# Kernel optimization log

Hardware: AMD Instinct MI355X
Metric: run time of the kernel (lower is better)

The kernel has to match this reference:

```python
import jax, jax.numpy as jnp
import numpy as np

WINDOW = 12
NUM_HEADS = 16

def window_partition(x, ws):
    b, h, w, c = x.shape
    x = x.reshape(b, h // ws, ws, w // ws, ws, c)
    return x.transpose(0, 1, 3, 2, 4, 5).reshape(-1, ws, ws, c)

def window_reverse(windows, ws, h, w):
    c = windows.shape[-1]
    x = windows.reshape(-1, h // ws, w // ws, ws, ws, c)
    return x.transpose(0, 1, 3, 2, 4, 5).reshape(-1, h, w, c)

def setup_inputs() -> dict:
    key = jax.random.key(0)
    ks = jax.random.split(key, 5)
    dim = 512
    hidden_states = jax.random.normal(ks[0], (8, 48, 48, dim), dtype=jnp.float32)
    qkv_w = jax.random.normal(ks[1], (dim, 3 * dim), dtype=jnp.float32) * 0.02
    qkv_b = jnp.zeros((3 * dim,), dtype=jnp.float32)
    proj_w = jax.random.normal(ks[2], (dim, dim), dtype=jnp.float32) * 0.02
    proj_b = jnp.zeros((dim,), dtype=jnp.float32)
    return {"hidden_states": hidden_states, "qkv_w": qkv_w, "qkv_b": qkv_b,
            "proj_w": proj_w, "proj_b": proj_b}

def reference(hidden_states, qkv_w, qkv_b, proj_w, proj_b):
    b, h, w, c = hidden_states.shape
    ws = WINDOW
    nh = NUM_HEADS
    hd = c // nh
    scale = hd ** -0.5
    pad_r = (ws - w % ws) % ws
    pad_b = (ws - h % ws) % ws
    x = jnp.pad(hidden_states, ((0, 0), (0, pad_b), (0, pad_r), (0, 0)))
    ph, pw = x.shape[1], x.shape[2]
    # [nW, ws*ws, C]
    xw = window_partition(x, ws).reshape(-1, ws * ws, c)
    nw, nt, _ = xw.shape
    qkv = (xw @ qkv_w + qkv_b).reshape(nw, nt, 3, nh, hd)
    qkv = qkv.transpose(2, 0, 3, 1, 4)  # [3, nW, nh, nt, hd]
    q, k, v = qkv[0], qkv[1], qkv[2]
    scores = jnp.einsum('wnqd,wnkd->wnqk', q, k) * scale
    attn = jax.nn.softmax(scores, axis=-1)
    out = jnp.einsum('wnqk,wnkd->wnqd', attn, v)  # [nW, nh, nt, hd]
    out = out.transpose(0, 2, 1, 3).reshape(nw, nt, c)
    out = out @ proj_w + proj_b
    out = out.reshape(-1, ws, ws, c)
    out = window_reverse(out, ws, ph, pw)
    out = out[:, :h, :w, :]
    return out.reshape(b, h * w, c)
```

## Files before the change

### kernel.cpp

```cpp
#include <hip/hip_runtime.h>
#include <hip/hip_bf16.h>


typedef unsigned short u16;
typedef unsigned int u32;
typedef __attribute__((ext_vector_type(4))) float f32x4;
typedef __attribute__((ext_vector_type(8))) short short8;

#define MFMA16(a, b, c) __builtin_amdgcn_mfma_f32_16x16x32_bf16(a, b, c, 0, 0, 0)

__device__ __forceinline__ u16 f2b(float f) {
  __hip_bfloat16 h = __float2bfloat16(f);
  return *reinterpret_cast<u16*>(&h);
}

__global__ void prep_x_kernel(const float* __restrict__ x, u16* __restrict__ xw) {
  int c = blockIdx.x * 256 + threadIdx.x;
  int r = c >> 6;
  int colb = (c & 63) << 3;
  int win = r / 144, tok = r - win * 144;
  int b = win >> 4, wh = (win >> 2) & 3, ww = win & 3;
  int i = tok / 12, j = tok - i * 12;
  const float* src = x + ((size_t)((b * 48 + wh * 12 + i) * 48 + ww * 12 + j)) * 512 + colb;
  float4 a0 = *(const float4*)(src);
  float4 a1 = *(const float4*)(src + 4);
  short8 o;
  o[0] = (short)f2b(a0.x); o[1] = (short)f2b(a0.y); o[2] = (short)f2b(a0.z); o[3] = (short)f2b(a0.w);
  o[4] = (short)f2b(a1.x); o[5] = (short)f2b(a1.y); o[6] = (short)f2b(a1.z); o[7] = (short)f2b(a1.w);
  *reinterpret_cast<short8*>(xw + (size_t)r * 512 + colb) = o;
}

__global__ void prep_wt_kernel(const float* __restrict__ w, u16* __restrict__ wt,
                               int K, int N) {
  int t = blockIdx.x * 256 + threadIdx.x;
  int nchunks = N >> 3;
  if (t >= K * nchunks) return;
  int k = t / nchunks;
  int n0 = (t - k * nchunks) << 3;
  const float* src = w + (size_t)k * N + n0;
  float4 a0 = *(const float4*)(src);
  float4 a1 = *(const float4*)(src + 4);
  float v[8] = {a0.x, a0.y, a0.z, a0.w, a1.x, a1.y, a1.z, a1.w};
#pragma unroll
  for (int j = 0; j < 8; j++) wt[(size_t)(n0 + j) * K + k] = f2b(v[j]);
}

template <int EPI>
__global__ __launch_bounds__(256) void gemm_bt_kernel(
    const u16* __restrict__ A, const u16* __restrict__ BT,
    const float* __restrict__ bias,
    u16* __restrict__ outb, float* __restrict__ outf,
    int M, int N, int K) {
  __shared__ __align__(16) u16 sA[128 * 64];
  __shared__ __align__(16) u16 sB[128 * 64];
  const int tid = threadIdx.x;
  const int wave = tid >> 6;
  const int lane = tid & 63;
  const int bm = blockIdx.x;
  const int bn = blockIdx.y;
  const int wr = (wave >> 1) << 6;
  const int wc = (wave & 1) << 6;
  const int l15 = lane & 15;
  const int lhi = lane >> 4;

  f32x4 acc[4][4];
  const f32x4 fzero = {0.f, 0.f, 0.f, 0.f};
#pragma unroll
  for (int i = 0; i < 4; i++)
#pragma unroll
    for (int j = 0; j < 4; j++) acc[i][j] = fzero;

  const int srow = lane >> 3;
  const int scol = (lane & 7) << 3;
  const u16* Abase = A + (size_t)(bm * 128) * K;
  const u16* Bbase = BT + (size_t)(bn * 128) * K;

  for (int k0 = 0; k0 < K; k0 += 64) {
#pragma unroll
    for (int i = 0; i < 4; ++i) {
      const int chunk = wave * 4 + i;
      const int row = chunk * 8 + srow;
      __builtin_amdgcn_global_load_lds(
          (const __attribute__((address_space(1))) u32*)(Abase + (size_t)row * K + k0 + scol),
          (__attribute__((address_space(3))) u32*)(sA + chunk * 512), 16, 0, 0);
      __builtin_amdgcn_global_load_lds(
          (const __attribute__((address_space(1))) u32*)(Bbase + (size_t)row * K + k0 + scol),
          (__attribute__((address_space(3))) u32*)(sB + chunk * 512), 16, 0, 0);
    }
    __syncthreads();

    short8 af[4][2], bfr[4][2];
#pragma unroll
    for (int t = 0; t < 4; t++) {
#pragma unroll
      for (int kk = 0; kk < 2; kk++) {
        af[t][kk]  = *reinterpret_cast<const short8*>(sA + (wr + t * 16 + l15) * 64 + kk * 32 + lhi * 8);
        bfr[t][kk] = *reinterpret_cast<const short8*>(sB + (wc + t * 16 + l15) * 64 + kk * 32 + lhi * 8);
      }
    }
#pragma unroll
    for (int kk = 0; kk < 2; kk++)
#pragma unroll
      for (int i = 0; i < 4; i++)
#pragma unroll
        for (int j = 0; j < 4; j++)
          acc[i][j] = MFMA16(af[i][kk], bfr[j][kk], acc[i][j]);
    __syncthreads();
  }

#pragma unroll
  for (int i = 0; i < 4; i++) {
    const int rowbase = bm * 128 + wr + i * 16 + lhi * 4;
#pragma unroll
    for (int j = 0; j < 4; j++) {
      const int col = bn * 128 + wc + j * 16 + l15;
      const float bv = bias[col];
#pragma unroll
      for (int r = 0; r < 4; r++) {
        float v = acc[i][j][r] + bv;
        int row = rowbase + r;
        if (EPI == 0) {
          outb[(size_t)row * N + col] = f2b(v);
        } else {
          int win = row / 144, tok = row - win * 144;
          int b = win >> 4, wh = (win >> 2) & 3, ww = win & 3;
          int ii = tok / 12, jj = tok - ii * 12;
          size_t o = ((size_t)b * 2304 + (wh * 12 + ii) * 48 + (ww * 12 + jj)) * 512 + col;
          outf[o] = v;
        }
      }
    }
  }
}

__global__ __launch_bounds__(192) void attn_kernel(const u16* __restrict__ qkv,
                                                   u16* __restrict__ outb) {
  constexpr int PSTR = 168;
  __shared__ __align__(16) u16 sP[3 * 48 * PSTR];
  __shared__ __align__(16) u16 sVT[32 * PSTR];
  const int tid = threadIdx.x;
  const int wave = tid >> 6;
  const int lane = tid & 63;
  const int l15 = lane & 15;
  const int lhi = lane >> 4;
  const int win = blockIdx.x;
  const int head = blockIdx.y;
  const size_t base = ((size_t)win * 144) * 1536 + head * 32;
  const u16* Q = qkv + base;
  const u16* Kp = qkv + base + 512;
  const u16* V = qkv + base + 1024;
  constexpr float SCALE = 0.17677669529663687f;
  const f32x4 fzero = {0.f, 0.f, 0.f, 0.f};

  for (int t = tid; t < 576; t += 192) {
    int tok = t >> 2, dblk = t & 3;
    short8 v = *reinterpret_cast<const short8*>(V + (size_t)tok * 1536 + dblk * 8);
#pragma unroll
    for (int j = 0; j < 8; j++) sVT[(dblk * 8 + j) * PSTR + tok] = (u16)v[j];
  }
  for (int t = tid; t < 512; t += 192) {
    int d = t >> 4, cc = 144 + (t & 15);
    sVT[d * PSTR + cc] = 0;
  }
  u16* sPw = sP + wave * 48 * PSTR;
  for (int t = lane; t < 768; t += 64) {
    int rr = t >> 4, cc = 144 + (t & 15);
    sPw[rr * PSTR + cc] = 0;
  }

  short8 qa[3];
#pragma unroll
  for (int mt = 0; mt < 3; mt++) {
    int row = wave * 48 + mt * 16 + l15;
    qa[mt] = *reinterpret_cast<const short8*>(Q + (size_t)row * 1536 + lhi * 8);
  }

  f32x4 s[3][9];
#pragma unroll
  for (int nt = 0; nt < 9; nt++) {
    int ctok = nt * 16 + l15;
    short8 kb = *reinterpret_cast<const short8*>(Kp + (size_t)ctok * 1536 + lhi * 8);
#pragma unroll
    for (int mt = 0; mt < 3; mt++) s[mt][nt] = MFMA16(qa[mt], kb, fzero);
  }

#pragma unroll
  for (int mt = 0; mt < 3; mt++) {
#pragma unroll
    for (int r = 0; r < 4; r++) {
      float m = -1e30f;
#pragma unroll
      for (int nt = 0; nt < 9; nt++) m = fmaxf(m, s[mt][nt][r]);
#pragma unroll
      for (int off = 1; off < 16; off <<= 1) m = fmaxf(m, __shfl_xor(m, off, 64));
      float p[9], sum = 0.f;
#pragma unroll
      for (int nt = 0; nt < 9; nt++) {
        p[nt] = __expf((s[mt][nt][r] - m) * SCALE);
        sum += p[nt];
      }
#pragma unroll
      for (int off = 1; off < 16; off <<= 1) sum += __shfl_xor(sum, off, 64);
      float inv = 1.f / sum;
      int prow = mt * 16 + lhi * 4 + r;
#pragma unroll
      for (int nt = 0; nt < 9; nt++)
        sPw[prow * PSTR + nt * 16 + l15] = f2b(p[nt] * inv);
    }
  }

  __syncthreads();

  f32x4 o[3][2];
#pragma unroll
  for (int mt = 0; mt < 3; mt++)
#pragma unroll
    for (int nt = 0; nt < 2; nt++) o[mt][nt] = fzero;
#pragma unroll
  for (int kk = 0; kk < 5; kk++) {
    short8 pa[3];
#pragma unroll
    for (int mt = 0; mt < 3; mt++)
      pa[mt] = *reinterpret_cast<const short8*>(sPw + (mt * 16 + l15) * PSTR + kk * 32 + lhi * 8);
#pragma unroll
    for (int nt = 0; nt < 2; nt++) {
      short8 vb = *reinterpret_cast<const short8*>(sVT + (nt * 16 + l15) * PSTR + kk * 32 + lhi * 8);
#pragma unroll
      for (int mt = 0; mt < 3; mt++) o[mt][nt] = MFMA16(pa[mt], vb, o[mt][nt]);
    }
  }

  const int rowb = win * 144 + wave * 48;
#pragma unroll
  for (int mt = 0; mt < 3; mt++) {
#pragma unroll
    for (int nt = 0; nt < 2; nt++) {
      int col = head * 32 + nt * 16 + l15;
#pragma unroll
      for (int r = 0; r < 4; r++) {
        int row = rowb + mt * 16 + lhi * 4 + r;
        outb[(size_t)row * 512 + col] = f2b(o[mt][nt][r]);
      }
    }
  }
}

extern "C" void kernel_launch(void* const* d_in, const int* in_sizes, int n_in,
                              void* d_out, int out_size, void* d_ws, size_t ws_size,
                              hipStream_t stream) {
  const float* x      = (const float*)d_in[0];
  const float* qkv_w  = (const float*)d_in[1];
  const float* qkv_b  = (const float*)d_in[2];
  const float* proj_w = (const float*)d_in[3];
  const float* proj_b = (const float*)d_in[4];
  float* out = (float*)d_out;

  u16* xw     = (u16*)d_ws;
  u16* qkvT   = xw + (size_t)18432 * 512;
  u16* projT  = qkvT + (size_t)1536 * 512;
  u16* qkvout = projT + (size_t)512 * 512;
  u16* attno  = qkvout + (size_t)18432 * 1536;

  prep_x_kernel<<<4608, 256, 0, stream>>>(x, xw);
  prep_wt_kernel<<<384, 256, 0, stream>>>(qkv_w, qkvT, 512, 1536);
  prep_wt_kernel<<<128, 256, 0, stream>>>(proj_w, projT, 512, 512);

  gemm_bt_kernel<0><<<dim3(144, 12), 256, 0, stream>>>(
      xw, qkvT, qkv_b, qkvout, nullptr, 18432, 1536, 512);

  attn_kernel<<<dim3(128, 16), 192, 0, stream>>>(qkvout, attno);

  gemm_bt_kernel<1><<<dim3(144, 4), 256, 0, stream>>>(
      attno, projT, proj_b, nullptr, out, 18432, 512, 512);
}
```

Baseline: 226.9 us.

## Swizzle GEMM LDS tiles and stream attention per row-tile to cut LDS and registers

The GEMM now XOR-swizzles the 16-byte chunk column by row when writing to and reading from LDS, which is meant to avoid bank conflicts on the MFMA operand loads. The attention kernel computes QK, softmax and PV for one 16-row tile at a time, reusing a per-wave P buffer one third the size. This reduces LDS footprint and live score registers, which may allow more blocks per CU. It also switches to exp2f with a prescaled log2e constant. Reusing the P buffer relies on intra-wave ordering of LDS writes and reads with no barrier, which is a correctness risk.

```diff
diff --git a/kernel.cpp b/kernel.cpp
--- a/kernel.cpp
+++ b/kernel.cpp
@@ -71,7 +71,7 @@
     for (int j = 0; j < 4; j++) acc[i][j] = fzero;
 
   const int srow = lane >> 3;
-  const int scol = (lane & 7) << 3;
+  const int scol = (((lane & 7) ^ srow) << 3);
   const u16* Abase = A + (size_t)(bm * 128) * K;
   const u16* Bbase = BT + (size_t)(bn * 128) * K;
 
@@ -94,8 +94,12 @@
     for (int t = 0; t < 4; t++) {
 #pragma unroll
       for (int kk = 0; kk < 2; kk++) {
-        af[t][kk]  = *reinterpret_cast<const short8*>(sA + (wr + t * 16 + l15) * 64 + kk * 32 + lhi * 8);
-        bfr[t][kk] = *reinterpret_cast<const short8*>(sB + (wc + t * 16 + l15) * 64 + kk * 32 + lhi * 8);
+        const int rA = wr + t * 16 + l15;
+        const int rB = wc + t * 16 + l15;
+        const int cA = (kk * 32 + lhi * 8) ^ ((rA & 7) << 3);
+        const int cB = (kk * 32 + lhi * 8) ^ ((rB & 7) << 3);
+        af[t][kk]  = *reinterpret_cast<const short8*>(sA + rA * 64 + cA);
+        bfr[t][kk] = *reinterpret_cast<const short8*>(sB + rB * 64 + cB);
       }
     }
 #pragma unroll
@@ -136,8 +140,8 @@
 __global__ __launch_bounds__(192) void attn_kernel(const u16* __restrict__ qkv,
                                                    u16* __restrict__ outb) {
   constexpr int PSTR = 168;
-  __shared__ __align__(16) u16 sP[3 * 48 * PSTR];
   __shared__ __align__(16) u16 sVT[32 * PSTR];
+  __shared__ __align__(16) u16 sP[3 * 16 * PSTR];
   const int tid = threadIdx.x;
   const int wave = tid >> 6;
   const int lane = tid & 63;
@@ -149,7 +153,7 @@
   const u16* Q = qkv + base;
   const u16* Kp = qkv + base + 512;
   const u16* V = qkv + base + 1024;
-  constexpr float SCALE = 0.17677669529663687f;
+  constexpr float SC2 = 0.25509915922608635f;
   const f32x4 fzero = {0.f, 0.f, 0.f, 0.f};
 
   for (int t = tid; t < 576; t += 192) {
@@ -162,10 +166,12 @@
     int d = t >> 4, cc = 144 + (t & 15);
     sVT[d * PSTR + cc] = 0;
   }
-  u16* sPw = sP + wave * 48 * PSTR;
-  for (int t = lane; t < 768; t += 64) {
-    int rr = t >> 4, cc = 144 + (t & 15);
-    sPw[rr * PSTR + cc] = 0;
+  u16* sPw = sP + wave * 16 * PSTR;
+  {
+    for (int t = lane; t < 256; t += 64) {
+      int rr = t >> 4, cc = 144 + (t & 15);
+      sPw[rr * PSTR + cc] = 0;
+    }
   }
 
   short8 qa[3];
@@ -174,59 +180,57 @@
     int row = wave * 48 + mt * 16 + l15;
     qa[mt] = *reinterpret_cast<const short8*>(Q + (size_t)row * 1536 + lhi * 8);
   }
-
-  f32x4 s[3][9];
+  short8 kb[9];
 #pragma unroll
   for (int nt = 0; nt < 9; nt++) {
     int ctok = nt * 16 + l15;
-    short8 kb = *reinterpret_cast<const short8*>(Kp + (size_t)ctok * 1536 + lhi * 8);
-#pragma unroll
-    for (int mt = 0; mt < 3; mt++) s[mt][nt] = MFMA16(qa[mt], kb, fzero);
-  }
+    kb[nt] = *reinterpret_cast<const short8*>(Kp + (size_t)ctok * 1536 + lhi * 8);
+  }
+
+  __syncthreads();
+
+  f32x4 o[3][2];
+#pragma unroll
+  for (int mt = 0; mt < 3; mt++)
+#pragma unroll
+    for (int nt = 0; nt < 2; nt++) o[mt][nt] = fzero;
 
 #pragma unroll
   for (int mt = 0; mt < 3; mt++) {
+    f32x4 s[9];
+#pragma unroll
+    for (int nt = 0; nt < 9; nt++) s[nt] = MFMA16(qa[mt], kb[nt], fzero);
+
 #pragma unroll
     for (int r = 0; r < 4; r++) {
       float m = -1e30f;
 #pragma unroll
-      for (int nt = 0; nt < 9; nt++) m = fmaxf(m, s[mt][nt][r]);
+      for (int nt = 0; nt < 9; nt++) m = fmaxf(m, s[nt][r]);
 #pragma unroll
       for (int off = 1; off < 16; off <<= 1) m = fmaxf(m, __shfl_xor(m, off, 64));
       float p[9], sum = 0.f;
 #pragma unroll
       for (int nt = 0; nt < 9; nt++) {
-        p[nt] = __expf((s[mt][nt][r] - m) * SCALE);
+        p[nt] = exp2f((s[nt][r] - m) * SC2);
         sum += p[nt];
       }
 #pragma unroll
       for (int off = 1; off < 16; off <<= 1) sum += __shfl_xor(sum, off, 64);
       float inv = 1.f / sum;
-      int prow = mt * 16 + lhi * 4 + r;
+      int prow = lhi * 4 + r;
 #pragma unroll
       for (int nt = 0; nt < 9; nt++)
         sPw[prow * PSTR + nt * 16 + l15] = f2b(p[nt] * inv);
     }
-  }
-
-  __syncthreads();
-
-  f32x4 o[3][2];
-#pragma unroll
-  for (int mt = 0; mt < 3; mt++)
-#pragma unroll
-    for (int nt = 0; nt < 2; nt++) o[mt][nt] = fzero;
-#pragma unroll
-  for (int kk = 0; kk < 5; kk++) {
-    short8 pa[3];
-#pragma unroll
-    for (int mt = 0; mt < 3; mt++)
-      pa[mt] = *reinterpret_cast<const short8*>(sPw + (mt * 16 + l15) * PSTR + kk * 32 + lhi * 8);
-#pragma unroll
-    for (int nt = 0; nt < 2; nt++) {
-      short8 vb = *reinterpret_cast<const short8*>(sVT + (nt * 16 + l15) * PSTR + kk * 32 + lhi * 8);
-#pragma unroll
-      for (int mt = 0; mt < 3; mt++) o[mt][nt] = MFMA16(pa[mt], vb, o[mt][nt]);
+
+#pragma unroll
+    for (int kk = 0; kk < 5; kk++) {
+      short8 pa = *reinterpret_cast<const short8*>(sPw + l15 * PSTR + kk * 32 + lhi * 8);
+#pragma unroll
+      for (int nt = 0; nt < 2; nt++) {
+        short8 vb = *reinterpret_cast<const short8*>(sVT + (nt * 16 + l15) * PSTR + kk * 32 + lhi * 8);
+        o[mt][nt] = MFMA16(pa, vb, o[mt][nt]);
+      }
     }
   }
 
```

Result: faster. 209.7 us (-7.6%).
